# Kernel optimization log

Hardware: AMD Instinct MI355X
Metric: run time of the kernel (lower is better)

Reference implementation:

```python
import jax, jax.numpy as jnp
import numpy as np

B, T, H_DIM, N_HEADS, FACTOR = 1, 2048, 2048, 16, 2
KEY_DIM = H_DIM // N_HEADS          # 128
V_DIM = H_DIM * FACTOR              # 4096
HEAD_DIM = V_DIM // N_HEADS         # 256
SCALING = KEY_DIM ** -0.5
EPS = 1e-6


def rotate_every_two(x):
    x1 = x[..., ::2]
    x2 = x[..., 1::2]
    return jnp.stack([-x2, x1], axis=-1).reshape(x.shape)


def theta_shift(x, sin, cos):
    return x * cos + rotate_every_two(x) * sin


def setup_inputs() -> dict:
    key = jax.random.key(0)
    ks = jax.random.split(key, 11)
    s = 0.02  # xavier-ish init scale
    inp = {
        'hidden_states': jax.random.normal(ks[0], (B, T, H_DIM), jnp.float32),
        'Wq': jax.random.normal(ks[1], (H_DIM, H_DIM), jnp.float32) * s,
        'bq': jnp.zeros((H_DIM,), jnp.float32),
        'Wk': jax.random.normal(ks[2], (H_DIM, H_DIM), jnp.float32) * s,
        'bk': jnp.zeros((H_DIM,), jnp.float32),
        'Wv': jax.random.normal(ks[3], (H_DIM, V_DIM), jnp.float32) * s,
        'bv': jnp.zeros((V_DIM,), jnp.float32),
        'Wg': jax.random.normal(ks[4], (H_DIM, V_DIM), jnp.float32) * s,
        'bg': jnp.zeros((V_DIM,), jnp.float32),
        'Wo': jax.random.normal(ks[5], (V_DIM, H_DIM), jnp.float32) * s,
        'bo': jnp.zeros((H_DIM,), jnp.float32),
    }
    # --- RetNetRelPos (parallel mode), as in syncdoth/RetNet ---
    angle = 1.0 / (10000 ** np.linspace(0, 1, KEY_DIM // 2))
    angle = np.repeat(angle, 2)                      # [key_dim]
    index = np.arange(T)
    inp['sin'] = jnp.asarray(np.sin(index[:, None] * angle[None, :]).astype(np.float32))
    inp['cos'] = jnp.asarray(np.cos(index[:, None] * angle[None, :]).astype(np.float32))
    decay = np.log(1 - 2.0 ** (-5 - np.arange(N_HEADS, dtype=np.float64)))  # [h], negative
    diff = index[:, None] - index[None, :]           # [T,T]
    tri = diff >= 0                                  # causal mask
    expo = decay[:, None, None] * np.where(tri, diff, 0)[None]  # [h,T,T]
    mask = np.where(tri[None], np.exp(expo), 0.0)
    mask = mask / np.sqrt(mask.sum(-1, keepdims=True))
    inp['decay_mask'] = jnp.asarray(mask[None].astype(np.float32))  # [1,h,T,T]
    return inp


def _msr_forward(hidden_states, sin, cos, decay_mask,
                 Wq, bq, Wk, bk, Wv, bv, Wg, bg, Wo, bo):
    Bsz, Tlen, _ = hidden_states.shape
    q = hidden_states @ Wq + bq                      # [B,T,H]
    k = hidden_states @ Wk + bk
    v = hidden_states @ Wv + bv                      # [B,T,V_DIM]
    g = hidden_states @ Wg + bg
    # split heads -> [B,h,T,dim]
    q = q.reshape(Bsz, Tlen, N_HEADS, KEY_DIM).transpose(0, 2, 1, 3)
    k = k.reshape(Bsz, Tlen, N_HEADS, KEY_DIM).transpose(0, 2, 1, 3)
    v = v.reshape(Bsz, Tlen, N_HEADS, HEAD_DIM).transpose(0, 2, 1, 3)
    k = k * SCALING
    qr = theta_shift(q, sin, cos)                    # sin/cos broadcast over B,h
    kr = theta_shift(k, sin, cos)
    # parallel retention: QK^T scaled by decay mask, row-normalized (detached denom)
    retention = jnp.einsum('bhsk,bhtk->bhst', qr, kr) * decay_mask
    denom = jnp.clip(jnp.abs(jax.lax.stop_gradient(retention).sum(-1, keepdims=True)), 1.0, None)
    retention = retention / denom
    out = jnp.einsum('bhst,bhtd->bshd', retention, v)  # [B,T,h,head_dim]
    # group_norm: LayerNorm over head_dim, eps=1e-6, no affine
    mu = out.mean(-1, keepdims=True)
    var = out.var(-1, keepdims=True)
    normed = ((out - mu) / jnp.sqrt(var + EPS)).reshape(Bsz, Tlen, V_DIM)
    gated = jax.nn.silu(g) * normed
    return gated @ Wo + bo                           # [B,T,H]


def reference(hidden_states, sin, cos, decay_mask,
              Wq, bq, Wk, bk, Wv, bv, Wg, bg, Wo, bo):
    return _msr_forward(hidden_states, sin, cos, decay_mask,
                        Wq, bq, Wk, bk, Wv, bv, Wg, bg, Wo, bo)
```

## Files before the change

### kernel.cpp

```cpp
#include <hip/hip_runtime.h>
#include <hip/hip_bf16.h>

typedef __hip_bfloat16 bf16;
typedef __attribute__((ext_vector_type(8))) __bf16 bf16x8;
typedef __attribute__((ext_vector_type(4))) float f32x4;

constexpr int TT = 2048;
constexpr int HD = 2048;
constexpr int VD = 4096;
constexpr int KD = 128;
constexpr int NH = 16;
constexpr int DH = 256;
constexpr float K_SCALING = 0.08838834764831845f;

__device__ __forceinline__ bf16 f2bf(float x) { return __float2bfloat16(x); }
__device__ __forceinline__ unsigned short f2bfu(float x) {
    bf16 b = __float2bfloat16(x);
    return *reinterpret_cast<unsigned short*>(&b);
}
__device__ __forceinline__ float bf2f(unsigned short u) {
    unsigned int x = ((unsigned int)u) << 16;
    return __uint_as_float(x);
}

__global__ __launch_bounds__(256) void transpose_all_k(
    const float* __restrict__ Wq, const float* __restrict__ Wk,
    const float* __restrict__ Wv, const float* __restrict__ Wg,
    const float* __restrict__ Wo, bf16* __restrict__ Wcat, bf16* __restrict__ WoT,
    const float* __restrict__ hidden, bf16* __restrict__ hb)
{
    __shared__ unsigned short sT[64 * 72];
    int t2 = blockIdx.x;
    if (t2 >= 8192) {
        const int b = t2 - 8192;
        const size_t base = (size_t)b * 8192;
#pragma unroll
        for (int j = 0; j < 8; ++j) {
            const size_t i = base + j * 1024 + threadIdx.x * 4;
            float4 v = *(const float4*)(hidden + i);
            bf16 tmp[4] = {f2bf(v.x), f2bf(v.y), f2bf(v.z), f2bf(v.w)};
            *(uint2*)(hb + i) = *(const uint2*)tmp;
        }
        return;
    }
    const float* src;
    bf16* dst;
    int R, C;
    if (t2 < 1024)      { src = Wq; dst = Wcat;                     R = 2048; C = 2048; }
    else if (t2 < 2048) { src = Wk; dst = Wcat + (size_t)2048 * HD; R = 2048; C = 2048; t2 -= 1024; }
    else if (t2 < 4096) { src = Wv; dst = Wcat + (size_t)4096 * HD; R = 2048; C = 4096; t2 -= 2048; }
    else if (t2 < 6144) { src = Wg; dst = Wcat + (size_t)8192 * HD; R = 2048; C = 4096; t2 -= 4096; }
    else                { src = Wo; dst = WoT;                      R = 4096; C = 2048; t2 -= 6144; }
    const int xt = C >> 6;
    const int x0 = (t2 % xt) * 64;
    const int y0 = (t2 / xt) * 64;

    const int t = threadIdx.x;
    {
        const int r = t >> 2;
        const int c0 = (t & 3) << 4;
        const float* s = src + (size_t)(y0 + r) * C + x0 + c0;
        unsigned short e[16];
#pragma unroll
        for (int j = 0; j < 4; ++j) {
            float4 v = *(const float4*)(s + j * 4);
            e[j * 4 + 0] = f2bfu(v.x);
            e[j * 4 + 1] = f2bfu(v.y);
            e[j * 4 + 2] = f2bfu(v.z);
            e[j * 4 + 3] = f2bfu(v.w);
        }
#pragma unroll
        for (int i = 0; i < 16; ++i) {
            const int c = c0 + i;
            sT[c * 72 + (r ^ (((c >> 3) & 7) << 3))] = e[i];
        }
    }
    __syncthreads();
    {
        const int c = t >> 2;
        const int r0 = (t & 3) << 4;
        const int xs = ((c >> 3) & 7) << 3;
#pragma unroll
        for (int s2 = 0; s2 < 16; s2 += 8) {
            bf16x8 v = *(const bf16x8*)&sT[c * 72 + ((r0 + s2) ^ xs)];
            *(bf16x8*)&dst[(size_t)(x0 + c) * R + y0 + r0 + s2] = v;
        }
    }
}

#define GLL(gptr, lptr) __builtin_amdgcn_global_load_lds( \
    (const __attribute__((address_space(1))) void*)(gptr), \
    (__attribute__((address_space(3))) void*)(lptr), 16, 0, 0)

#define STA(bufs, u, k1) GLL(gA0 + (size_t)((u) * 64) * HD + (k1), sA + (bufs) + (u) * 4096 + tid * 8)
#define STB(bufs, u, k1) GLL(gB0 + (size_t)((u) * 64) * HD + (k1), sB + (bufs) + (u) * 4096 + tid * 8)

#define WAIT6 asm volatile("s_waitcnt vmcnt(6)" ::: "memory")
#define WAIT0V asm volatile("s_waitcnt vmcnt(0)" ::: "memory")
#define MEMF asm volatile("" ::: "memory")
#define BAR __builtin_amdgcn_s_barrier()

#define LDA(dst, cb, qm) \
    _Pragma("unroll") for (int mi = 0; mi < 4; ++mi) { \
        const int r_ = wr * 128 + (qm) * 64 + mi * 16 + lr; \
        _Pragma("unroll") for (int ks = 0; ks < 2; ++ks) \
            dst[mi][ks] = *(const bf16x8*)&sA[(cb) + r_ * 64 + (((ks * 4 + g) ^ (lr & 7)) << 3)]; \
    }

#define LDB01(dst, cb) \
    _Pragma("unroll") for (int ni = 0; ni < 2; ++ni) { \
        const int n_ = wcn * 48 + ni * 16 + lr; \
        _Pragma("unroll") for (int ks = 0; ks < 2; ++ks) \
            dst[ni][ks] = *(const bf16x8*)&sB[(cb) + n_ * 64 + (((ks * 4 + g) ^ (lr & 7)) << 3)]; \
    }

#define LDB2(dst, cb) { \
        const int n_ = wcn * 48 + 32 + lr; \
        _Pragma("unroll") for (int ks = 0; ks < 2; ++ks) \
            dst[ks] = *(const bf16x8*)&sB[(cb) + n_ * 64 + (((ks * 4 + g) ^ (lr & 7)) << 3)]; \
    }

#define Q00 __builtin_amdgcn_s_setprio(1); \
    _Pragma("unroll") for (int mi = 0; mi < 4; ++mi) \
        _Pragma("unroll") for (int ni = 0; ni < 2; ++ni) \
            _Pragma("unroll") for (int ks = 0; ks < 2; ++ks) \
                acc[mi][ni] = __builtin_amdgcn_mfma_f32_16x16x32_bf16(ra0[mi][ks], rb[ni][ks], acc[mi][ni], 0, 0, 0); \
    __builtin_amdgcn_s_setprio(0);
#define Q10 __builtin_amdgcn_s_setprio(1); \
    _Pragma("unroll") for (int mi = 0; mi < 4; ++mi) \
        _Pragma("unroll") for (int ni = 0; ni < 2; ++ni) \
            _Pragma("unroll") for (int ks = 0; ks < 2; ++ks) \
                acc[4 + mi][ni] = __builtin_amdgcn_mfma_f32_16x16x32_bf16(ra1[mi][ks], rb[ni][ks], acc[4 + mi][ni], 0, 0, 0); \
    __builtin_amdgcn_s_setprio(0);
#define Q11 __builtin_amdgcn_s_setprio(1); \
    _Pragma("unroll") for (int mi = 0; mi < 4; ++mi) \
        _Pragma("unroll") for (int ks = 0; ks < 2; ++ks) \
            acc[4 + mi][2] = __builtin_amdgcn_mfma_f32_16x16x32_bf16(ra1[mi][ks], rb2[ks], acc[4 + mi][2], 0, 0, 0); \
    __builtin_amdgcn_s_setprio(0);
#define Q01 __builtin_amdgcn_s_setprio(1); \
    _Pragma("unroll") for (int mi = 0; mi < 4; ++mi) \
        _Pragma("unroll") for (int ks = 0; ks < 2; ++ks) \
            acc[mi][2] = __builtin_amdgcn_mfma_f32_16x16x32_bf16(ra0[mi][ks], rb2[ks], acc[mi][2], 0, 0, 0); \
    __builtin_amdgcn_s_setprio(0);

__global__ __launch_bounds__(512, 2) void gemm_qkvg_k(
    const bf16* __restrict__ Ag, const bf16* __restrict__ Bg,
    const float* __restrict__ bq, const float* __restrict__ bk,
    const float* __restrict__ bvp, const float* __restrict__ bg,
    const float* __restrict__ sinT, const float* __restrict__ cosT,
    bf16* __restrict__ qr, bf16* __restrict__ kr,
    bf16* __restrict__ vT, bf16* __restrict__ sg)
{
    __shared__ unsigned short sA[2 * 256 * 64];
    __shared__ unsigned short sB[2 * 192 * 64];
    constexpr int BUFA = 16384, BUFB = 12288;

    const int tid = threadIdx.x;
    const int lane = tid & 63;
    const int w = tid >> 6;
    const int wr = w >> 2;
    const int wcn = w & 3;
    const int lr = lane & 15;
    const int g = lane >> 4;

    const int flat = blockIdx.x;
    const int swz = (flat & 7) * 64 + (flat >> 3);
    const int brow = (swz & 7) * 256;
    const int bcol = (swz >> 3) * 192;

    const bf16* gA0 = Ag + (size_t)(brow + (tid >> 3)) * HD + (((tid & 7) ^ ((tid >> 3) & 7)) << 3);
    const bf16* gB0 = Bg + (size_t)(bcol + (tid >> 3)) * HD + (((tid & 7) ^ ((tid >> 3) & 7)) << 3);

    f32x4 acc[8][3] = {};
    bf16x8 ra0[4][2], ra1[4][2], rb[2][2], rb2[2];

    STA(0, 0, 0); STA(0, 1, 0); STA(0, 2, 0); STA(0, 3, 0);
    STB(0, 0, 0); STB(0, 1, 0); STB(0, 2, 0);
    STA(BUFA, 0, 64); STA(BUFA, 1, 64); STA(BUFA, 2, 64); STA(BUFA, 3, 64);
    STB(BUFB, 0, 64); STB(BUFB, 1, 64);
    WAIT6; MEMF; BAR;

    for (int I = 0; I < 15; ++I) {
        const int kB1 = I * 128 + 64;
        const int kN2 = I * 128 + 128;
        const int kN3 = I * 128 + 192;
        LDA(ra0, 0, 0) LDB01(rb, 0)
        STB(BUFB, 2, kB1);
        MEMF; BAR; Q00 BAR;
        LDA(ra1, 0, 1)
        STA(0, 0, kN2); STA(0, 2, kN2);
        MEMF; BAR; Q10 BAR;
        LDB2(rb2, 0)
        STA(0, 1, kN2); STA(0, 3, kN2);
        MEMF; BAR; Q11 BAR;
        STB(0, 0, kN2); STB(0, 1, kN2);
        WAIT6; MEMF; BAR; Q01 BAR;
        LDA(ra0, BUFA, 0) LDB01(rb, BUFB)
        STB(0, 2, kN2);
        MEMF; BAR; Q00 BAR;
        LDA(ra1, BUFA, 1)
        STA(BUFA, 0, kN3); STA(BUFA, 2, kN3);
        MEMF; BAR; Q10 BAR;
        LDB2(rb2, BUFB)
        STA(BUFA, 1, kN3); STA(BUFA, 3, kN3);
        MEMF; BAR; Q11 BAR;
        STB(BUFB, 0, kN3); STB(BUFB, 1, kN3);
        WAIT6; MEMF; BAR; Q01 BAR;
    }
    {
        LDA(ra0, 0, 0) LDB01(rb, 0)
        STB(BUFB, 2, 1984);
        MEMF; BAR; Q00 BAR;
        LDA(ra1, 0, 1)
        MEMF; BAR; Q10 BAR;
        LDB2(rb2, 0)
        MEMF; BAR; Q11 BAR;
        WAIT0V; MEMF; BAR; Q01 BAR;
        LDA(ra0, BUFA, 0) LDB01(rb, BUFB)
        Q00
        LDA(ra1, BUFA, 1)
        Q10
        LDB2(rb2, BUFB)
        Q11
        Q01
    }

#pragma unroll
    for (int M = 0; M < 8; ++M) {
        const int row = brow + wr * 128 + (M >> 2) * 64 + (M & 3) * 16 + g * 4;
#pragma unroll
        for (int f = 0; f < 3; ++f) {
            const int colg = bcol + wcn * 48 + f * 16 + lr;
            if (colg < 4096) {
                const bool isK = (colg >= 2048);
                const int col = colg - (isK ? 2048 : 0);
                const float bvv = (isK ? bk : bq)[col];
                const float scale = isK ? K_SCALING : 1.f;
                bf16* outb = isK ? kr : qr;
                const int d = col & (KD - 1);
#pragma unroll
                for (int r = 0; r < 4; ++r) {
                    float v = (acc[M][f][r] + bvv) * scale;
                    float o = __shfl_xor(v, 1);
                    float rot = (col & 1) ? o : -o;
                    outb[(size_t)(row + r) * HD + col] =
                        f2bf(v * cosT[(row + r) * KD + d] + rot * sinT[(row + r) * KD + d]);
                }
            } else if (colg < 8192) {
                const int col = colg - 4096;
                const float bvv = bvp[col];
                bf16 tmp[4];
#pragma unroll
                for (int r = 0; r < 4; ++r)
                    tmp[r] = f2bf(acc[M][f][r] + bvv);
                *(uint2*)&vT[(size_t)col * TT + row] = *(const uint2*)tmp;
            } else {
                const int col = colg - 8192;
                const float bvv = bg[col];
#pragma unroll
                for (int r = 0; r < 4; ++r) {
                    float v = acc[M][f][r] + bvv;
                    sg[(size_t)(row + r) * VD + col] = f2bf(v / (1.f + __expf(-v)));
                }
            }
        }
    }
}

#define OSTA(bufs, u, k1) GLL(oA0 + (size_t)((u) * 64) * VD + (k1), sA + (bufs) + (u) * 4096 + tid * 8)
#define OSTB(bufs, u, k1) GLL(oB0 + (size_t)((u) * 64) * VD + (k1), sB + (bufs) + (u) * 4096 + tid * 8)

#define OLDA(dst, cb, qm) \
    _Pragma("unroll") for (int mi = 0; mi < 4; ++mi) { \
        const int r_ = wr * 128 + (qm) * 64 + mi * 16 + lr; \
        _Pragma("unroll") for (int ks = 0; ks < 2; ++ks) \
            dst[mi][ks] = *(const bf16x8*)&sA[(cb) + r_ * 64 + (((ks * 4 + g) ^ (lr & 7)) << 3)]; \
    }

#define OLDB(dst, cb, qn) \
    _Pragma("unroll") for (int ni = 0; ni < 2; ++ni) { \
        const int n_ = wcn * 64 + (qn) * 32 + ni * 16 + lr; \
        _Pragma("unroll") for (int ks = 0; ks < 2; ++ks) \
            dst[ni][ks] = *(const bf16x8*)&sB[(cb) + n_ * 64 + (((ks * 4 + g) ^ (lr & 7)) << 3)]; \
    }

#define OQ(qm, qn, RA, RB) __builtin_amdgcn_s_setprio(1); \
    _Pragma("unroll") for (int mi = 0; mi < 4; ++mi) \
        _Pragma("unroll") for (int ni = 0; ni < 2; ++ni) \
            _Pragma("unroll") for (int ks = 0; ks < 2; ++ks) \
                acc[(qm) * 4 + mi][(qn) * 2 + ni] = __builtin_amdgcn_mfma_f32_16x16x32_bf16( \
                    RA[mi][ks], RB[ni][ks], acc[(qm) * 4 + mi][(qn) * 2 + ni], 0, 0, 0); \
    __builtin_amdgcn_s_setprio(0);

__global__ __launch_bounds__(512, 2) void gemm_out_k(
    const bf16* __restrict__ Ag, const bf16* __restrict__ Bg,
    float* __restrict__ outp)
{
    __shared__ unsigned short sA[2 * 256 * 64];
    __shared__ unsigned short sB[2 * 256 * 64];
    constexpr int BUF1 = 16384;

    const int tid = threadIdx.x;
    const int lane = tid & 63;
    const int w = tid >> 6;
    const int wr = w >> 2;
    const int wcn = w & 3;
    const int lr = lane & 15;
    const int g = lane >> 4;

    const int flat = blockIdx.x;
    const int swz = (flat & 7) * 32 + (flat >> 3);
    const int z = swz >> 6;
    const int t64 = swz & 63;
    const int brow = (t64 & 7) * 256;
    const int bcol = (t64 >> 3) * 256;
    const int kbase = z * 1024;

    const bf16* oA0 = Ag + (size_t)(brow + (tid >> 3)) * VD + kbase + (((tid & 7) ^ ((tid >> 3) & 7)) << 3);
    const bf16* oB0 = Bg + (size_t)(bcol + (tid >> 3)) * VD + kbase + (((tid & 7) ^ ((tid >> 3) & 7)) << 3);

    f32x4 acc[8][4] = {};
    bf16x8 ra0[4][2], ra1[4][2], rb[2][2];

    OSTA(0, 0, 0); OSTA(0, 1, 0); OSTA(0, 2, 0); OSTA(0, 3, 0);
    OSTB(0, 0, 0); OSTB(0, 1, 0); OSTB(0, 2, 0); OSTB(0, 3, 0);
    OSTA(BUF1, 0, 64); OSTA(BUF1, 2, 64); OSTA(BUF1, 1, 64); OSTA(BUF1, 3, 64);
    OSTB(BUF1, 0, 64); OSTB(BUF1, 1, 64);
    WAIT6; MEMF; BAR;

    for (int I = 0; I < 7; ++I) {
        const int kB1 = I * 128 + 64;
        const int kN2 = I * 128 + 128;
        const int kN3 = I * 128 + 192;
        OLDA(ra0, 0, 0) OLDB(rb, 0, 0)
        OSTB(BUF1, 2, kB1); OSTB(BUF1, 3, kB1);
        MEMF; BAR; OQ(0, 0, ra0, rb) BAR;
        OLDA(ra1, 0, 1)
        OSTA(0, 0, kN2); OSTA(0, 2, kN2);
        MEMF; BAR; OQ(1, 0, ra1, rb) BAR;
        OLDB(rb, 0, 1)
        OSTA(0, 1, kN2); OSTA(0, 3, kN2);
        MEMF; BAR; OQ(1, 1, ra1, rb) BAR;
        OSTB(0, 0, kN2); OSTB(0, 1, kN2);
        WAIT6; MEMF; BAR; OQ(0, 1, ra0, rb) BAR;
        OLDA(ra0, BUF1, 0) OLDB(rb, BUF1, 0)
        OSTB(0, 2, kN2); OSTB(0, 3, kN2);
        MEMF; BAR; OQ(0, 0, ra0, rb) BAR;
        OLDA(ra1, BUF1, 1)
        OSTA(BUF1, 0, kN3); OSTA(BUF1, 2, kN3);
        MEMF; BAR; OQ(1, 0, ra1, rb) BAR;
        OLDB(rb, BUF1, 1)
        OSTA(BUF1, 1, kN3); OSTA(BUF1, 3, kN3);
        MEMF; BAR; OQ(1, 1, ra1, rb) BAR;
        OSTB(BUF1, 0, kN3); OSTB(BUF1, 1, kN3);
        WAIT6; MEMF; BAR; OQ(0, 1, ra0, rb) BAR;
    }
    {
        OLDA(ra0, 0, 0) OLDB(rb, 0, 0)
        OSTB(BUF1, 2, 960); OSTB(BUF1, 3, 960);
        MEMF; BAR; OQ(0, 0, ra0, rb) BAR;
        OLDA(ra1, 0, 1)
        MEMF; BAR; OQ(1, 0, ra1, rb) BAR;
        OLDB(rb, 0, 1)
        MEMF; BAR; OQ(1, 1, ra1, rb) BAR;
        WAIT0V; MEMF; BAR; OQ(0, 1, ra0, rb) BAR;
        OLDA(ra0, BUF1, 0) OLDB(rb, BUF1, 0)
        OQ(0, 0, ra0, rb)
        OLDA(ra1, BUF1, 1)
        OQ(1, 0, ra1, rb)
        OLDB(rb, BUF1, 1)
        OQ(1, 1, ra1, rb)
        OQ(0, 1, ra0, rb)
    }

    float* op = outp + (size_t)z * TT * HD;
#pragma unroll
    for (int M = 0; M < 8; ++M) {
        const int row = brow + wr * 128 + (M >> 2) * 64 + (M & 3) * 16 + g * 4;
#pragma unroll
        for (int N = 0; N < 4; ++N) {
            const int col = bcol + wcn * 64 + (N >> 1) * 32 + (N & 1) * 16 + lr;
#pragma unroll
            for (int r = 0; r < 4; ++r)
                op[(size_t)(row + r) * HD + col] = acc[M][N][r];
        }
    }
}

__global__ __launch_bounds__(256) void combine_out_k(const float* __restrict__ outp,
                                                     const float* __restrict__ bias,
                                                     float* __restrict__ out) {
    const size_t i = ((size_t)blockIdx.x * 256 + threadIdx.x) * 4;
    const size_t P = (size_t)TT * HD;
    float4 a = *(const float4*)(outp + i);
    float4 b = *(const float4*)(outp + P + i);
    float4 c = *(const float4*)(outp + 2 * P + i);
    float4 d = *(const float4*)(outp + 3 * P + i);
    float4 bi = *(const float4*)(bias + (i & (HD - 1)));
    float4 o;
    o.x = (a.x + b.x) + (c.x + d.x) + bi.x;
    o.y = (a.y + b.y) + (c.y + d.y) + bi.y;
    o.z = (a.z + b.z) + (c.z + d.z) + bi.z;
    o.w = (a.w + b.w) + (c.w + d.w) + bi.w;
    *(float4*)(out + i) = o;
}

__global__ __launch_bounds__(512) void retention_fused_k(
    const bf16* __restrict__ qr, const bf16* __restrict__ kr,
    const bf16* __restrict__ vT,
    bf16* __restrict__ po0, bf16* __restrict__ po1,
    float* __restrict__ pr0, float* __restrict__ pr1)
{
    __shared__ unsigned short P_lds[2 * 128 * 128];
    __shared__ float rsum_lds[4][128];

    const int tid = threadIdx.x;
    const int lane = tid & 63;
    const int wid = tid >> 6;
    const int wr64 = (wid >> 2) * 64;
    const int wc = wid & 3;
    const int lr = lane & 15;
    const int g = lane >> 4;
    const int lk = g << 3;
    const int pidx = blockIdx.x;
    const int parity = blockIdx.y;
    const int h = blockIdx.z;

    const float decay = logf(1.f - exp2f(-5.f - (float)h));
    bf16* __restrict__ po = parity ? po1 : po0;
    float* __restrict__ pr = parity ? pr1 : pr0;

    const int swzA = (lr & 7) << 3;

    const float bfac0 = __expf(decay * (float)(-(wc * 32 + lr)));
    const float bfac1 = __expf(decay * (float)(-(wc * 32 + 16 + lr)));
    const float astep = __expf(decay * -256.f);

    for (int sec = 0; sec < 2; ++sec) {
        const int qb = sec ? (15 - pidx) : pidx;
        const int qrow0 = qb * 128;

        bf16x8 af[4][4];
#pragma unroll
        for (int mi = 0; mi < 4; ++mi)
#pragma unroll
            for (int ks = 0; ks < 4; ++ks)
                af[mi][ks] = *(const bf16x8*)&qr[(size_t)(qrow0 + wr64 + mi * 16 + lr) * HD +
                                                 h * KD + ks * 32 + lk];

        f32x4 acc_o[4][4] = {};
        float rs[4][4] = {};
        float aexp[4][4];
#pragma unroll
        for (int mi = 0; mi < 4; ++mi)
#pragma unroll
            for (int r = 0; r < 4; ++r) {
                const int row_l = wr64 + mi * 16 + g * 4 + r;
                aexp[mi][r] = __expf(decay * (float)(qrow0 + row_l - parity * 128));
            }

        int pb = 0;
        for (int tb = parity; tb <= qb; tb += 2) {
            const int t0 = tb * 128;

            f32x4 acc_p[4][2] = {};
#pragma unroll
            for (int ks = 0; ks < 4; ++ks) {
                const bf16x8 b0 = *(const bf16x8*)&kr[(size_t)(t0 + wc * 32 + lr) * HD +
                                                      h * KD + ks * 32 + lk];
                const bf16x8 b1 = *(const bf16x8*)&kr[(size_t)(t0 + wc * 32 + 16 + lr) * HD +
                                                      h * KD + ks * 32 + lk];
#pragma unroll
                for (int mi = 0; mi < 4; ++mi) {
                    acc_p[mi][0] = __builtin_amdgcn_mfma_f32_16x16x32_bf16(af[mi][ks], b0, acc_p[mi][0], 0, 0, 0);
                    acc_p[mi][1] = __builtin_amdgcn_mfma_f32_16x16x32_bf16(af[mi][ks], b1, acc_p[mi][1], 0, 0, 0);
                }
            }

#pragma unroll
            for (int mi = 0; mi < 4; ++mi) {
#pragma unroll
                for (int r = 0; r < 4; ++r) {
                    const int rl = g * 4 + r;
                    const int row_l = wr64 + mi * 16 + rl;
                    const int srel = qrow0 + row_l - t0;
                    const float a = aexp[mi][r];
                    const float p0 = (wc * 32 + lr <= srel) ? acc_p[mi][0][r] * a * bfac0 : 0.f;
                    const float p1 = (wc * 32 + 16 + lr <= srel) ? acc_p[mi][1][r] * a * bfac1 : 0.f;
                    const int sw = (rl & 7) << 3;
                    P_lds[pb + row_l * 128 + ((wc * 32 + lr) ^ sw)] = f2bfu(p0);
                    P_lds[pb + row_l * 128 + ((wc * 32 + 16 + lr) ^ sw)] = f2bfu(p1);
                    rs[mi][r] += p0 + p1;
                    aexp[mi][r] = a * astep;
                }
            }
            __syncthreads();

#pragma unroll
            for (int ks2 = 0; ks2 < 4; ++ks2) {
                bf16x8 a2[4], b2[4];
#pragma unroll
                for (int mi = 0; mi < 4; ++mi)
                    a2[mi] = *(const bf16x8*)&P_lds[pb + (wr64 + mi * 16 + lr) * 128 +
                                                    ((ks2 * 32 + lk) ^ swzA)];
#pragma unroll
                for (int ni = 0; ni < 4; ++ni)
                    b2[ni] = *(const bf16x8*)&vT[(size_t)(h * DH + wc * 64 + ni * 16 + lr) * TT +
                                                 t0 + ks2 * 32 + lk];
#pragma unroll
                for (int mi = 0; mi < 4; ++mi)
#pragma unroll
                    for (int ni = 0; ni < 4; ++ni)
                        acc_o[mi][ni] = __builtin_amdgcn_mfma_f32_16x16x32_bf16(a2[mi], b2[ni], acc_o[mi][ni], 0, 0, 0);
            }
            pb ^= 16384;
        }

#pragma unroll
        for (int mi = 0; mi < 4; ++mi)
#pragma unroll
            for (int r = 0; r < 4; ++r) {
                float v = rs[mi][r];
                v += __shfl_xor(v, 1);
                v += __shfl_xor(v, 2);
                v += __shfl_xor(v, 4);
                v += __shfl_xor(v, 8);
                if (lr == 0) rsum_lds[wc][wr64 + mi * 16 + g * 4 + r] = v;
            }
        __syncthreads();
        if (tid < 128)
            pr[(size_t)h * TT + qrow0 + tid] =
                rsum_lds[0][tid] + rsum_lds[1][tid] + rsum_lds[2][tid] + rsum_lds[3][tid];

#pragma unroll
        for (int mi = 0; mi < 4; ++mi)
#pragma unroll
            for (int ni = 0; ni < 4; ++ni)
#pragma unroll
                for (int r = 0; r < 4; ++r) {
                    const int row_l = wr64 + mi * 16 + g * 4 + r;
                    const int col = wc * 64 + ni * 16 + lr;
                    po[(size_t)(qrow0 + row_l) * VD + h * DH + col] = f2bf(acc_o[mi][ni][r]);
                }
        __syncthreads();
    }
}

__global__ __launch_bounds__(256) void ln_gate_k(const bf16* __restrict__ po0,
                                                 const bf16* __restrict__ po1,
                                                 const float* __restrict__ pr0,
                                                 const float* __restrict__ pr1,
                                                 const bf16* __restrict__ sg,
                                                 bf16* __restrict__ gated) {
    const int tid = threadIdx.x;
    const int lane = tid & 63;
    const size_t ridx = (size_t)blockIdx.x * 4 + (tid >> 6);
    const int h = (int)(ridx & 15);
    const int s = (int)(ridx >> 4);

    const float decay = logf(1.f - exp2f(-5.f - (float)h));
    const float Sm = -expm1f(decay * (float)(s + 1)) * exp2f(5.f + (float)h);
    const float norm = rsqrtf(Sm);
    const float raw = pr0[(size_t)h * TT + s] + pr1[(size_t)h * TT + s];
    const float scale = norm / fmaxf(1.f, fabsf(raw * norm));

    unsigned short ua[4], ub[4];
    *(uint2*)ua = *(const uint2*)(po0 + ridx * 256 + lane * 4);
    *(uint2*)ub = *(const uint2*)(po1 + ridx * 256 + lane * 4);
    float vv[4];
#pragma unroll
    for (int i = 0; i < 4; ++i)
        vv[i] = (bf2f(ua[i]) + bf2f(ub[i])) * scale;
    float sm = vv[0] + vv[1] + vv[2] + vv[3];
    float sq = vv[0] * vv[0] + vv[1] * vv[1] + vv[2] * vv[2] + vv[3] * vv[3];
#pragma unroll
    for (int o = 1; o < 64; o <<= 1) {
        sm += __shfl_xor(sm, o);
        sq += __shfl_xor(sq, o);
    }
    const float mu = sm * (1.f / 256.f);
    const float var = sq * (1.f / 256.f) - mu * mu;
    const float rstd = rsqrtf(var + 1e-6f);
    const bf16* sgp = sg + ridx * 256 + lane * 4;
    bf16* gp = gated + ridx * 256 + lane * 4;
    bf16 ob[4];
#pragma unroll
    for (int i = 0; i < 4; ++i)
        ob[i] = f2bf((vv[i] - mu) * rstd * __bfloat162float(sgp[i]));
    *(uint2*)gp = *(const uint2*)ob;
}

extern "C" void kernel_launch(void* const* d_in, const int* in_sizes, int n_in,
                              void* d_out, int out_size, void* d_ws, size_t ws_size,
                              hipStream_t stream) {
    const float* hidden = (const float*)d_in[0];
    const float* Wq = (const float*)d_in[1];
    const float* bq = (const float*)d_in[2];
    const float* Wk = (const float*)d_in[3];
    const float* bk = (const float*)d_in[4];
    const float* Wv = (const float*)d_in[5];
    const float* bvp = (const float*)d_in[6];
    const float* Wg = (const float*)d_in[7];
    const float* bg = (const float*)d_in[8];
    const float* Wo = (const float*)d_in[9];
    const float* bo = (const float*)d_in[10];
    const float* sinT = (const float*)d_in[11];
    const float* cosT = (const float*)d_in[12];
    float* out = (float*)d_out;

    char* p = (char*)d_ws;
    bf16* hb = (bf16*)p;    p += (size_t)TT * HD * 2;
    bf16* Wcat = (bf16*)p;  p += (size_t)(HD + HD + VD + VD) * HD * 2;
    bf16* WoT = (bf16*)p;   p += (size_t)HD * VD * 2;
    bf16* qr = (bf16*)p;    p += (size_t)TT * HD * 2;
    bf16* kr = (bf16*)p;    p += (size_t)TT * HD * 2;
    bf16* vT = (bf16*)p;    p += (size_t)VD * TT * 2;
    bf16* sg = (bf16*)p;    p += (size_t)TT * VD * 2;
    bf16* po0 = (bf16*)p;   p += (size_t)TT * VD * 2;
    bf16* po1 = (bf16*)p;   p += (size_t)TT * VD * 2;
    float* pr0 = (float*)p; p += (size_t)NH * TT * 4;
    float* pr1 = (float*)p; p += (size_t)NH * TT * 4;
    bf16* gated = (bf16*)p; p += (size_t)TT * VD * 2;
    float* outp = (float*)p; p += (size_t)4 * TT * HD * 4;

    transpose_all_k<<<8704, 256, 0, stream>>>(Wq, Wk, Wv, Wg, Wo, Wcat, WoT, hidden, hb);

    gemm_qkvg_k<<<512, 512, 0, stream>>>(hb, Wcat, bq, bk, bvp, bg, sinT, cosT,
                                         qr, kr, vT, sg);

    retention_fused_k<<<dim3(8, 2, NH), 512, 0, stream>>>(qr, kr, vT, po0, po1, pr0, pr1);

    ln_gate_k<<<TT * NH / 4, 256, 0, stream>>>(po0, po1, pr0, pr1, sg, gated);
    gemm_out_k<<<256, 512, 0, stream>>>(gated, WoT, outp);
    combine_out_k<<<TT * HD / 1024, 256, 0, stream>>>(outp, bo, out);
}
```

Measured before the change: 313.9 us.

## Double retention kernel threads to 1024 and store split-K output partials as bf16

The retention kernel now runs 1024 threads per block, 16 waves each covering 32 query rows instead of 64. This halves per-wave accumulator state and adds waves to hide latency. As a trade-off, Q fragments are reloaded from global memory on every key tile rather than held in registers. Separately, the four split-K partial outputs of the output projection are written and read as bf16 instead of fp32, halving that intermediate traffic at the cost of extra rounding error in the final sum.

Measured after the change: 433.7 us. +38.2%, slower.

```diff
diff --git a/kernel.cpp b/kernel.cpp
--- a/kernel.cpp
+++ b/kernel.cpp
@@ -294,7 +294,7 @@
 
 __global__ __launch_bounds__(512, 2) void gemm_out_k(
     const bf16* __restrict__ Ag, const bf16* __restrict__ Bg,
-    float* __restrict__ outp)
+    bf16* __restrict__ outp)
 {
     __shared__ unsigned short sA[2 * 256 * 64];
     __shared__ unsigned short sB[2 * 256 * 64];
@@ -373,7 +373,7 @@
         OQ(0, 1, ra0, rb)
     }
 
-    float* op = outp + (size_t)z * TT * HD;
+    bf16* op = outp + (size_t)z * TT * HD;
 #pragma unroll
     for (int M = 0; M < 8; ++M) {
         const int row = brow + wr * 128 + (M >> 2) * 64 + (M & 3) * 16 + g * 4;
@@ -382,30 +382,31 @@
             const int col = bcol + wcn * 64 + (N >> 1) * 32 + (N & 1) * 16 + lr;
 #pragma unroll
             for (int r = 0; r < 4; ++r)
-                op[(size_t)(row + r) * HD + col] = acc[M][N][r];
+                op[(size_t)(row + r) * HD + col] = f2bf(acc[M][N][r]);
         }
     }
 }
 
-__global__ __launch_bounds__(256) void combine_out_k(const float* __restrict__ outp,
+__global__ __launch_bounds__(256) void combine_out_k(const bf16* __restrict__ outp,
                                                      const float* __restrict__ bias,
                                                      float* __restrict__ out) {
     const size_t i = ((size_t)blockIdx.x * 256 + threadIdx.x) * 4;
     const size_t P = (size_t)TT * HD;
-    float4 a = *(const float4*)(outp + i);
-    float4 b = *(const float4*)(outp + P + i);
-    float4 c = *(const float4*)(outp + 2 * P + i);
-    float4 d = *(const float4*)(outp + 3 * P + i);
+    unsigned short a[4], b[4], c[4], d[4];
+    *(uint2*)a = *(const uint2*)(outp + i);
+    *(uint2*)b = *(const uint2*)(outp + P + i);
+    *(uint2*)c = *(const uint2*)(outp + 2 * P + i);
+    *(uint2*)d = *(const uint2*)(outp + 3 * P + i);
     float4 bi = *(const float4*)(bias + (i & (HD - 1)));
-    float4 o;
-    o.x = (a.x + b.x) + (c.x + d.x) + bi.x;
-    o.y = (a.y + b.y) + (c.y + d.y) + bi.y;
-    o.z = (a.z + b.z) + (c.z + d.z) + bi.z;
-    o.w = (a.w + b.w) + (c.w + d.w) + bi.w;
-    *(float4*)(out + i) = o;
-}
-
-__global__ __launch_bounds__(512) void retention_fused_k(
+    float o[4];
+#pragma unroll
+    for (int j = 0; j < 4; ++j)
+        o[j] = (bf2f(a[j]) + bf2f(b[j])) + (bf2f(c[j]) + bf2f(d[j]));
+    float4 ov = {o[0] + bi.x, o[1] + bi.y, o[2] + bi.z, o[3] + bi.w};
+    *(float4*)(out + i) = ov;
+}
+
+__global__ __launch_bounds__(1024, 4) void retention_fused_k(
     const bf16* __restrict__ qr, const bf16* __restrict__ kr,
     const bf16* __restrict__ vT,
     bf16* __restrict__ po0, bf16* __restrict__ po1,
@@ -417,7 +418,7 @@
     const int tid = threadIdx.x;
     const int lane = tid & 63;
     const int wid = tid >> 6;
-    const int wr64 = (wid >> 2) * 64;
+    const int wq32 = (wid >> 2) * 32;
     const int wc = wid & 3;
     const int lr = lane & 15;
     const int g = lane >> 4;
@@ -440,22 +441,14 @@
         const int qb = sec ? (15 - pidx) : pidx;
         const int qrow0 = qb * 128;
 
-        bf16x8 af[4][4];
-#pragma unroll
-        for (int mi = 0; mi < 4; ++mi)
-#pragma unroll
-            for (int ks = 0; ks < 4; ++ks)
-                af[mi][ks] = *(const bf16x8*)&qr[(size_t)(qrow0 + wr64 + mi * 16 + lr) * HD +
-                                                 h * KD + ks * 32 + lk];
-
-        f32x4 acc_o[4][4] = {};
-        float rs[4][4] = {};
-        float aexp[4][4];
-#pragma unroll
-        for (int mi = 0; mi < 4; ++mi)
+        f32x4 acc_o[2][4] = {};
+        float rs[2][4] = {};
+        float aexp[2][4];
+#pragma unroll
+        for (int mi = 0; mi < 2; ++mi)
 #pragma unroll
             for (int r = 0; r < 4; ++r) {
-                const int row_l = wr64 + mi * 16 + g * 4 + r;
+                const int row_l = wq32 + mi * 16 + g * 4 + r;
                 aexp[mi][r] = __expf(decay * (float)(qrow0 + row_l - parity * 128));
             }
 
@@ -463,26 +456,29 @@
         for (int tb = parity; tb <= qb; tb += 2) {
             const int t0 = tb * 128;
 
-            f32x4 acc_p[4][2] = {};
+            f32x4 acc_p[2][2] = {};
 #pragma unroll
             for (int ks = 0; ks < 4; ++ks) {
+                const bf16x8 a0 = *(const bf16x8*)&qr[(size_t)(qrow0 + wq32 + lr) * HD +
+                                                      h * KD + ks * 32 + lk];
+                const bf16x8 a1 = *(const bf16x8*)&qr[(size_t)(qrow0 + wq32 + 16 + lr) * HD +
+                                                      h * KD + ks * 32 + lk];
                 const bf16x8 b0 = *(const bf16x8*)&kr[(size_t)(t0 + wc * 32 + lr) * HD +
                                                       h * KD + ks * 32 + lk];
                 const bf16x8 b1 = *(const bf16x8*)&kr[(size_t)(t0 + wc * 32 + 16 + lr) * HD +
                                                       h * KD + ks * 32 + lk];
-#pragma unroll
-                for (int mi = 0; mi < 4; ++mi) {
-                    acc_p[mi][0] = __builtin_amdgcn_mfma_f32_16x16x32_bf16(af[mi][ks], b0, acc_p[mi][0], 0, 0, 0);
-                    acc_p[mi][1] = __builtin_amdgcn_mfma_f32_16x16x32_bf16(af[mi][ks], b1, acc_p[mi][1], 0, 0, 0);
-                }
+                acc_p[0][0] = __builtin_amdgcn_mfma_f32_16x16x32_bf16(a0, b0, acc_p[0][0], 0, 0, 0);
+                acc_p[0][1] = __builtin_amdgcn_mfma_f32_16x16x32_bf16(a0, b1, acc_p[0][1], 0, 0, 0);
+                acc_p[1][0] = __builtin_amdgcn_mfma_f32_16x16x32_bf16(a1, b0, acc_p[1][0], 0, 0, 0);
+                acc_p[1][1] = __builtin_amdgcn_mfma_f32_16x16x32_bf16(a1, b1, acc_p[1][1], 0, 0, 0);
             }
 
 #pragma unroll
-            for (int mi = 0; mi < 4; ++mi) {
+            for (int mi = 0; mi < 2; ++mi) {
 #pragma unroll
                 for (int r = 0; r < 4; ++r) {
                     const int rl = g * 4 + r;
-                    const int row_l = wr64 + mi * 16 + rl;
+                    const int row_l = wq32 + mi * 16 + rl;
                     const int srel = qrow0 + row_l - t0;
                     const float a = aexp[mi][r];
                     const float p0 = (wc * 32 + lr <= srel) ? acc_p[mi][0][r] * a * bfac0 : 0.f;
@@ -498,17 +494,17 @@
 
 #pragma unroll
             for (int ks2 = 0; ks2 < 4; ++ks2) {
-                bf16x8 a2[4], b2[4];
-#pragma unroll
-                for (int mi = 0; mi < 4; ++mi)
-                    a2[mi] = *(const bf16x8*)&P_lds[pb + (wr64 + mi * 16 + lr) * 128 +
+                bf16x8 a2[2], b2[4];
+#pragma unroll
+                for (int mi = 0; mi < 2; ++mi)
+                    a2[mi] = *(const bf16x8*)&P_lds[pb + (wq32 + mi * 16 + lr) * 128 +
                                                     ((ks2 * 32 + lk) ^ swzA)];
 #pragma unroll
                 for (int ni = 0; ni < 4; ++ni)
                     b2[ni] = *(const bf16x8*)&vT[(size_t)(h * DH + wc * 64 + ni * 16 + lr) * TT +
                                                  t0 + ks2 * 32 + lk];
 #pragma unroll
-                for (int mi = 0; mi < 4; ++mi)
+                for (int mi = 0; mi < 2; ++mi)
 #pragma unroll
                     for (int ni = 0; ni < 4; ++ni)
                         acc_o[mi][ni] = __builtin_amdgcn_mfma_f32_16x16x32_bf16(a2[mi], b2[ni], acc_o[mi][ni], 0, 0, 0);
@@ -517,7 +513,7 @@
         }
 
 #pragma unroll
-        for (int mi = 0; mi < 4; ++mi)
+        for (int mi = 0; mi < 2; ++mi)
 #pragma unroll
             for (int r = 0; r < 4; ++r) {
                 float v = rs[mi][r];
@@ -525,7 +521,7 @@
                 v += __shfl_xor(v, 2);
                 v += __shfl_xor(v, 4);
                 v += __shfl_xor(v, 8);
-                if (lr == 0) rsum_lds[wc][wr64 + mi * 16 + g * 4 + r] = v;
+                if (lr == 0) rsum_lds[wc][wq32 + mi * 16 + g * 4 + r] = v;
             }
         __syncthreads();
         if (tid < 128)
@@ -533,12 +529,12 @@
                 rsum_lds[0][tid] + rsum_lds[1][tid] + rsum_lds[2][tid] + rsum_lds[3][tid];
 
 #pragma unroll
-        for (int mi = 0; mi < 4; ++mi)
+        for (int mi = 0; mi < 2; ++mi)
 #pragma unroll
             for (int ni = 0; ni < 4; ++ni)
 #pragma unroll
                 for (int r = 0; r < 4; ++r) {
-                    const int row_l = wr64 + mi * 16 + g * 4 + r;
+                    const int row_l = wq32 + mi * 16 + g * 4 + r;
                     const int col = wc * 64 + ni * 16 + lr;
                     po[(size_t)(qrow0 + row_l) * VD + h * DH + col] = f2bf(acc_o[mi][ni][r]);
                 }
@@ -621,14 +617,14 @@
     float* pr0 = (float*)p; p += (size_t)NH * TT * 4;
     float* pr1 = (float*)p; p += (size_t)NH * TT * 4;
     bf16* gated = (bf16*)p; p += (size_t)TT * VD * 2;
-    float* outp = (float*)p; p += (size_t)4 * TT * HD * 4;
+    bf16* outp = (bf16*)p;  p += (size_t)4 * TT * HD * 2;
 
     transpose_all_k<<<8704, 256, 0, stream>>>(Wq, Wk, Wv, Wg, Wo, Wcat, WoT, hidden, hb);
 
     gemm_qkvg_k<<<512, 512, 0, stream>>>(hb, Wcat, bq, bk, bvp, bg, sinT, cosT,
                                          qr, kr, vT, sg);
 
-    retention_fused_k<<<dim3(8, 2, NH), 512, 0, stream>>>(qr, kr, vT, po0, po1, pr0, pr1);
+    retention_fused_k<<<dim3(8, 2, NH), 1024, 0, stream>>>(qr, kr, vT, po0, po1, pr0, pr1);
 
     ln_gate_k<<<TT * NH / 4, 256, 0, stream>>>(po0, po1, pr0, pr1, sg, gated);
     gemm_out_k<<<256, 512, 0, stream>>>(gated, WoT, outp);
```
